# Kernel tuning notes

Hardware: AMD Instinct MI355X
Metric: run time of the kernel (lower is better)

## Reference

```python
import jax, jax.numpy as jnp
import numpy as np

D = 3  # feature dim fixed by the module's Linear(3,3) layers
N = 6144

def _linear(x, w, b):
    # torch Linear: y = x @ W^T + b, W: [out,in]
    return x @ w.T + b

def setup_inputs() -> dict:
    key = jax.random.key(0)
    ks = jax.random.split(key, 20)
    lim = 1.0 / np.sqrt(D)  # torch default init bound
    def W(k):
        return jax.random.uniform(k, (D, D), jnp.float32, -lim, lim)
    def B(k):
        return jax.random.uniform(k, (D,), jnp.float32, -lim, lim)
    inp = {"x_data": jax.random.normal(ks[0], (N, D), jnp.float32)}
    names = ["q1", "q2", "q3", "q4", "k1", "k2", "v1", "v2", "b1b2"]
    for i, nm in enumerate(names):
        inp["w_" + nm] = W(ks[1 + 2 * i])
        inp["b_" + nm] = B(ks[2 + 2 * i])
    return inp

def reference(x_data, w_q1, b_q1, w_q2, b_q2, w_q3, b_q3, w_q4, b_q4,
              w_k1, b_k1, w_k2, b_k2, w_v1, b_v1, w_v2, b_v2, w_b1b2, b_b1b2):
    k1 = _linear(x_data, w_k1, b_k1)
    k2 = _linear(x_data, w_k2, b_k2)
    group1 = _linear(x_data, w_q1, b_q1) + _linear(x_data, w_q2, b_q2)
    group2 = _linear(x_data, w_q3, b_q3) + _linear(x_data, w_q4, b_q4)
    a1 = jax.nn.softmax(group1 @ k1.T, axis=1)  # [N, N]
    a2 = jax.nn.softmax(group2 @ k2.T, axis=1)  # [N, N]
    v1 = _linear(x_data, w_v1, b_v1)
    v2 = _linear(x_data, w_v2, b_v2)
    b = _linear(a1 @ v1 + a2 @ v2, w_b1b2, b_b1b2)  # [N, D]
    return (a1, b)
```

## Files before the change

### kernel.cpp

```cpp
#include <hip/hip_runtime.h>
#include <cstddef>

#define N_ROWS 6144
#define TR 8
#define NT 256
#define NBLK (N_ROWS / TR)
#define JT (NT * 4)
#define NIT (N_ROWS / JT)
#define L2E 1.44269504088896340736f

typedef float f32x4 __attribute__((ext_vector_type(4)));

#if __has_builtin(__builtin_amdgcn_exp2f)
#define EXP2F(x) __builtin_amdgcn_exp2f(x)
#else
#define EXP2F(x) exp2f(x)
#endif
#if __has_builtin(__builtin_amdgcn_logf)
#define LOG2F(x) __builtin_amdgcn_logf(x)
#else
#define LOG2F(x) log2f(x)
#endif

__device__ __forceinline__ float wredSum(float v) {
#pragma unroll
    for (int off = 32; off > 0; off >>= 1) v += __shfl_xor(v, off, 64);
    return v;
}

__global__ __launch_bounds__(NT, 2) void attn_fused(
    const float* __restrict__ x,
    const float* __restrict__ wq1, const float* __restrict__ bq1,
    const float* __restrict__ wq2, const float* __restrict__ bq2,
    const float* __restrict__ wq3, const float* __restrict__ bq3,
    const float* __restrict__ wq4, const float* __restrict__ bq4,
    const float* __restrict__ wk1, const float* __restrict__ bk1,
    const float* __restrict__ wk2, const float* __restrict__ bk2,
    const float* __restrict__ wv1, const float* __restrict__ bv1,
    const float* __restrict__ wv2, const float* __restrict__ bv2,
    const float* __restrict__ wb,  const float* __restrict__ bb,
    float* __restrict__ out)
{
    const int row0 = blockIdx.x * TR;
    const int tid  = threadIdx.x;
    const int wave = tid >> 6;
    const int lane = tid & 63;

    __shared__ float red[4][64];

    float wg1[9], wg2[9], bg1[3], bg2[3];
    float k1w[9], k2w[9], v1w[9], v2w[9];
    float k1b[3], k2b[3], v1b[3], v2b[3];
#pragma unroll
    for (int t = 0; t < 9; t++) {
        wg1[t] = (wq1[t] + wq2[t]) * L2E;
        wg2[t] = (wq3[t] + wq4[t]) * L2E;
        k1w[t] = wk1[t]; k2w[t] = wk2[t];
        v1w[t] = wv1[t]; v2w[t] = wv2[t];
    }
#pragma unroll
    for (int t = 0; t < 3; t++) {
        bg1[t] = (bq1[t] + bq2[t]) * L2E;
        bg2[t] = (bq3[t] + bq4[t]) * L2E;
        k1b[t] = bk1[t]; k2b[t] = bk2[t];
        v1b[t] = bv1[t]; v2b[t] = bv2[t];
    }

    float g1x[TR], g1y[TR], g1z[TR], g2x[TR], g2y[TR], g2z[TR];
#pragma unroll
    for (int r = 0; r < TR; r++) {
        const int i = row0 + r;
        const float x0 = x[3*i+0], x1 = x[3*i+1], x2 = x[3*i+2];
        g1x[r] = wg1[0]*x0 + wg1[1]*x1 + wg1[2]*x2 + bg1[0];
        g1y[r] = wg1[3]*x0 + wg1[4]*x1 + wg1[5]*x2 + bg1[1];
        g1z[r] = wg1[6]*x0 + wg1[7]*x1 + wg1[8]*x2 + bg1[2];
        g2x[r] = wg2[0]*x0 + wg2[1]*x1 + wg2[2]*x2 + bg2[0];
        g2y[r] = wg2[3]*x0 + wg2[4]*x1 + wg2[5]*x2 + bg2[1];
        g2z[r] = wg2[6]*x0 + wg2[7]*x1 + wg2[8]*x2 + bg2[2];
    }

    float l1[TR], l2[TR];
    float o1x[TR], o1y[TR], o1z[TR], o2x[TR], o2y[TR], o2z[TR];
#pragma unroll
    for (int r = 0; r < TR; r++) {
        l1[r]=0.f; l2[r]=0.f;
        o1x[r]=0.f; o1y[r]=0.f; o1z[r]=0.f;
        o2x[r]=0.f; o2y[r]=0.f; o2z[r]=0.f;
    }

    for (int it = 0; it < NIT; it++) {
        const int j0 = it * JT + tid * 4;
        const f32x4 xa = *(const f32x4*)(x + 3*j0);
        const f32x4 xb = *(const f32x4*)(x + 3*j0 + 4);
        const f32x4 xc = *(const f32x4*)(x + 3*j0 + 8);
        const float xs[12] = { xa.x, xa.y, xa.z, xa.w, xb.x, xb.y,
                               xb.z, xb.w, xc.x, xc.y, xc.z, xc.w };
#pragma unroll
        for (int jj = 0; jj < 4; jj++) {
            const float xx = xs[3*jj], xy = xs[3*jj+1], xz = xs[3*jj+2];
            const float k1x = k1w[0]*xx + k1w[1]*xy + k1w[2]*xz + k1b[0];
            const float k1y = k1w[3]*xx + k1w[4]*xy + k1w[5]*xz + k1b[1];
            const float k1z = k1w[6]*xx + k1w[7]*xy + k1w[8]*xz + k1b[2];
            const float k2x = k2w[0]*xx + k2w[1]*xy + k2w[2]*xz + k2b[0];
            const float k2y = k2w[3]*xx + k2w[4]*xy + k2w[5]*xz + k2b[1];
            const float k2z = k2w[6]*xx + k2w[7]*xy + k2w[8]*xz + k2b[2];
            const float v1x = v1w[0]*xx + v1w[1]*xy + v1w[2]*xz + v1b[0];
            const float v1y = v1w[3]*xx + v1w[4]*xy + v1w[5]*xz + v1b[1];
            const float v1z = v1w[6]*xx + v1w[7]*xy + v1w[8]*xz + v1b[2];
            const float v2x = v2w[0]*xx + v2w[1]*xy + v2w[2]*xz + v2b[0];
            const float v2y = v2w[3]*xx + v2w[4]*xy + v2w[5]*xz + v2b[1];
            const float v2z = v2w[6]*xx + v2w[7]*xy + v2w[8]*xz + v2b[2];
#pragma unroll
            for (int r = 0; r < TR; r++) {
                const float t1 = fmaf(g1z[r], k1z, fmaf(g1y[r], k1y, g1x[r]*k1x));
                const float t2 = fmaf(g2z[r], k2z, fmaf(g2y[r], k2y, g2x[r]*k2x));
                const float e1 = EXP2F(t1);
                const float e2 = EXP2F(t2);
                l1[r] += e1; l2[r] += e2;
                o1x[r] = fmaf(e1, v1x, o1x[r]);
                o1y[r] = fmaf(e1, v1y, o1y[r]);
                o1z[r] = fmaf(e1, v1z, o1z[r]);
                o2x[r] = fmaf(e2, v2x, o2x[r]);
                o2y[r] = fmaf(e2, v2y, o2y[r]);
                o2z[r] = fmaf(e2, v2z, o2z[r]);
            }
        }
    }

#pragma unroll
    for (int r = 0; r < TR; r++) {
        l1[r]  = wredSum(l1[r]);  l2[r]  = wredSum(l2[r]);
        o1x[r] = wredSum(o1x[r]); o1y[r] = wredSum(o1y[r]); o1z[r] = wredSum(o1z[r]);
        o2x[r] = wredSum(o2x[r]); o2y[r] = wredSum(o2y[r]); o2z[r] = wredSum(o2z[r]);
        if (lane == 0) {
            red[wave][r*8+0]=l1[r];  red[wave][r*8+1]=l2[r];
            red[wave][r*8+2]=o1x[r]; red[wave][r*8+3]=o1y[r]; red[wave][r*8+4]=o1z[r];
            red[wave][r*8+5]=o2x[r]; red[wave][r*8+6]=o2y[r]; red[wave][r*8+7]=o2z[r];
        }
    }
    __syncthreads();

    float c1p[TR];
#pragma unroll
    for (int r = 0; r < TR; r++) {
        const float l1t = red[0][r*8] + red[1][r*8] + red[2][r*8] + red[3][r*8];
        c1p[r] = -LOG2F(l1t);
    }

    for (int it = 0; it < NIT; it++) {
        const int j0 = it * JT + tid * 4;
        const f32x4 xa = *(const f32x4*)(x + 3*j0);
        const f32x4 xb = *(const f32x4*)(x + 3*j0 + 4);
        const f32x4 xc = *(const f32x4*)(x + 3*j0 + 8);
        const float xs[12] = { xa.x, xa.y, xa.z, xa.w, xb.x, xb.y,
                               xb.z, xb.w, xc.x, xc.y, xc.z, xc.w };
        float K1x[4], K1y[4], K1z[4];
#pragma unroll
        for (int jj = 0; jj < 4; jj++) {
            const float xx = xs[3*jj], xy = xs[3*jj+1], xz = xs[3*jj+2];
            K1x[jj] = k1w[0]*xx + k1w[1]*xy + k1w[2]*xz + k1b[0];
            K1y[jj] = k1w[3]*xx + k1w[4]*xy + k1w[5]*xz + k1b[1];
            K1z[jj] = k1w[6]*xx + k1w[7]*xy + k1w[8]*xz + k1b[2];
        }
#pragma unroll
        for (int r = 0; r < TR; r++) {
            f32x4 pv;
            pv.x = EXP2F(fmaf(g1z[r], K1z[0], fmaf(g1y[r], K1y[0], fmaf(g1x[r], K1x[0], c1p[r]))));
            pv.y = EXP2F(fmaf(g1z[r], K1z[1], fmaf(g1y[r], K1y[1], fmaf(g1x[r], K1x[1], c1p[r]))));
            pv.z = EXP2F(fmaf(g1z[r], K1z[2], fmaf(g1y[r], K1y[2], fmaf(g1x[r], K1x[2], c1p[r]))));
            pv.w = EXP2F(fmaf(g1z[r], K1z[3], fmaf(g1y[r], K1y[3], fmaf(g1x[r], K1x[3], c1p[r]))));
            __builtin_nontemporal_store(pv, (f32x4*)(out + (size_t)(row0 + r) * N_ROWS + j0));
        }
    }

    if (tid < TR) {
        const int r = tid;
        const float l1t = red[0][r*8+0]+red[1][r*8+0]+red[2][r*8+0]+red[3][r*8+0];
        const float l2t = red[0][r*8+1]+red[1][r*8+1]+red[2][r*8+1]+red[3][r*8+1];
        const float sx1 = red[0][r*8+2]+red[1][r*8+2]+red[2][r*8+2]+red[3][r*8+2];
        const float sy1 = red[0][r*8+3]+red[1][r*8+3]+red[2][r*8+3]+red[3][r*8+3];
        const float sz1 = red[0][r*8+4]+red[1][r*8+4]+red[2][r*8+4]+red[3][r*8+4];
        const float sx2 = red[0][r*8+5]+red[1][r*8+5]+red[2][r*8+5]+red[3][r*8+5];
        const float sy2 = red[0][r*8+6]+red[1][r*8+6]+red[2][r*8+6]+red[3][r*8+6];
        const float sz2 = red[0][r*8+7]+red[1][r*8+7]+red[2][r*8+7]+red[3][r*8+7];
        const float r1 = 1.0f / l1t, r2 = 1.0f / l2t;
        const float ox = sx1*r1 + sx2*r2;
        const float oy = sy1*r1 + sy2*r2;
        const float oz = sz1*r1 + sz2*r2;
        const float b0 = wb[0]*ox + wb[1]*oy + wb[2]*oz + bb[0];
        const float b1 = wb[3]*ox + wb[4]*oy + wb[5]*oz + bb[1];
        const float b2 = wb[6]*ox + wb[7]*oy + wb[8]*oz + bb[2];
        const size_t base = (size_t)N_ROWS * N_ROWS + (size_t)(row0 + r) * 3;
        out[base+0] = b0; out[base+1] = b1; out[base+2] = b2;
    }
}

extern "C" void kernel_launch(void* const* d_in, const int* in_sizes, int n_in,
                              void* d_out, int out_size, void* d_ws, size_t ws_size,
                              hipStream_t stream) {
    const float* x   = (const float*)d_in[0];
    const float* wq1 = (const float*)d_in[1];  const float* bq1 = (const float*)d_in[2];
    const float* wq2 = (const float*)d_in[3];  const float* bq2 = (const float*)d_in[4];
    const float* wq3 = (const float*)d_in[5];  const float* bq3 = (const float*)d_in[6];
    const float* wq4 = (const float*)d_in[7];  const float* bq4 = (const float*)d_in[8];
    const float* wk1 = (const float*)d_in[9];  const float* bk1 = (const float*)d_in[10];
    const float* wk2 = (const float*)d_in[11]; const float* bk2 = (const float*)d_in[12];
    const float* wv1 = (const float*)d_in[13]; const float* bv1 = (const float*)d_in[14];
    const float* wv2 = (const float*)d_in[15]; const float* bv2 = (const float*)d_in[16];
    const float* wb  = (const float*)d_in[17]; const float* bb  = (const float*)d_in[18];

    float* out = (float*)d_out;

    attn_fused<<<NBLK, NT, 0, stream>>>(
        x, wq1,bq1, wq2,bq2, wq3,bq3, wq4,bq4,
        wk1,bk1, wk2,bk2, wv1,bv1, wv2,bv2, wb, bb, out);
}
```

Baseline: 220.3 us.

## Split row tile into halves to overlap softmax stores with next-half reduction

Splits each block's 8 rows into two halves of 4. The reduction pass for the second half is fused with writing the normalized attention rows of the first half, so exp-heavy compute and the large nontemporal output stores interleave instead of running in separate phases. Register pressure per loop drops, but x is loaded and K/V recomputed in three passes with less row reuse, and an extra block barrier is added.

```diff
diff --git a/kernel.cpp b/kernel.cpp
--- a/kernel.cpp
+++ b/kernel.cpp
@@ -2,6 +2,7 @@
 #include <cstddef>
 
 #define N_ROWS 6144
+#define TRH 4
 #define TR 8
 #define NT 256
 #define NBLK (N_ROWS / TR)
@@ -46,7 +47,8 @@
     const int wave = tid >> 6;
     const int lane = tid & 63;
 
-    __shared__ float red[4][64];
+    __shared__ float redA[4][TRH * 8];
+    __shared__ float redB[4][TRH * 8];
 
     float wg1[9], wg2[9], bg1[3], bg2[3];
     float k1w[9], k2w[9], v1w[9], v2w[9];
@@ -79,10 +81,10 @@
         g2z[r] = wg2[6]*x0 + wg2[7]*x1 + wg2[8]*x2 + bg2[2];
     }
 
-    float l1[TR], l2[TR];
-    float o1x[TR], o1y[TR], o1z[TR], o2x[TR], o2y[TR], o2z[TR];
-#pragma unroll
-    for (int r = 0; r < TR; r++) {
+    float l1[TRH], l2[TRH];
+    float o1x[TRH], o1y[TRH], o1z[TRH], o2x[TRH], o2y[TRH], o2z[TRH];
+#pragma unroll
+    for (int r = 0; r < TRH; r++) {
         l1[r]=0.f; l2[r]=0.f;
         o1x[r]=0.f; o1y[r]=0.f; o1z[r]=0.f;
         o2x[r]=0.f; o2y[r]=0.f; o2z[r]=0.f;
@@ -111,7 +113,7 @@
             const float v2y = v2w[3]*xx + v2w[4]*xy + v2w[5]*xz + v2b[1];
             const float v2z = v2w[6]*xx + v2w[7]*xy + v2w[8]*xz + v2b[2];
 #pragma unroll
-            for (int r = 0; r < TR; r++) {
+            for (int r = 0; r < TRH; r++) {
                 const float t1 = fmaf(g1z[r], k1z, fmaf(g1y[r], k1y, g1x[r]*k1x));
                 const float t2 = fmaf(g2z[r], k2z, fmaf(g2y[r], k2y, g2x[r]*k2x));
                 const float e1 = EXP2F(t1);
@@ -128,61 +130,35 @@
     }
 
 #pragma unroll
-    for (int r = 0; r < TR; r++) {
+    for (int r = 0; r < TRH; r++) {
         l1[r]  = wredSum(l1[r]);  l2[r]  = wredSum(l2[r]);
         o1x[r] = wredSum(o1x[r]); o1y[r] = wredSum(o1y[r]); o1z[r] = wredSum(o1z[r]);
         o2x[r] = wredSum(o2x[r]); o2y[r] = wredSum(o2y[r]); o2z[r] = wredSum(o2z[r]);
         if (lane == 0) {
-            red[wave][r*8+0]=l1[r];  red[wave][r*8+1]=l2[r];
-            red[wave][r*8+2]=o1x[r]; red[wave][r*8+3]=o1y[r]; red[wave][r*8+4]=o1z[r];
-            red[wave][r*8+5]=o2x[r]; red[wave][r*8+6]=o2y[r]; red[wave][r*8+7]=o2z[r];
+            redA[wave][r*8+0]=l1[r];  redA[wave][r*8+1]=l2[r];
+            redA[wave][r*8+2]=o1x[r]; redA[wave][r*8+3]=o1y[r]; redA[wave][r*8+4]=o1z[r];
+            redA[wave][r*8+5]=o2x[r]; redA[wave][r*8+6]=o2y[r]; redA[wave][r*8+7]=o2z[r];
         }
     }
     __syncthreads();
 
-    float c1p[TR];
-#pragma unroll
-    for (int r = 0; r < TR; r++) {
-        const float l1t = red[0][r*8] + red[1][r*8] + red[2][r*8] + red[3][r*8];
-        c1p[r] = -LOG2F(l1t);
-    }
-
-    for (int it = 0; it < NIT; it++) {
-        const int j0 = it * JT + tid * 4;
-        const f32x4 xa = *(const f32x4*)(x + 3*j0);
-        const f32x4 xb = *(const f32x4*)(x + 3*j0 + 4);
-        const f32x4 xc = *(const f32x4*)(x + 3*j0 + 8);
-        const float xs[12] = { xa.x, xa.y, xa.z, xa.w, xb.x, xb.y,
-                               xb.z, xb.w, xc.x, xc.y, xc.z, xc.w };
-        float K1x[4], K1y[4], K1z[4];
-#pragma unroll
-        for (int jj = 0; jj < 4; jj++) {
-            const float xx = xs[3*jj], xy = xs[3*jj+1], xz = xs[3*jj+2];
-            K1x[jj] = k1w[0]*xx + k1w[1]*xy + k1w[2]*xz + k1b[0];
-            K1y[jj] = k1w[3]*xx + k1w[4]*xy + k1w[5]*xz + k1b[1];
-            K1z[jj] = k1w[6]*xx + k1w[7]*xy + k1w[8]*xz + k1b[2];
-        }
-#pragma unroll
-        for (int r = 0; r < TR; r++) {
-            f32x4 pv;
-            pv.x = EXP2F(fmaf(g1z[r], K1z[0], fmaf(g1y[r], K1y[0], fmaf(g1x[r], K1x[0], c1p[r]))));
-            pv.y = EXP2F(fmaf(g1z[r], K1z[1], fmaf(g1y[r], K1y[1], fmaf(g1x[r], K1x[1], c1p[r]))));
-            pv.z = EXP2F(fmaf(g1z[r], K1z[2], fmaf(g1y[r], K1y[2], fmaf(g1x[r], K1x[2], c1p[r]))));
-            pv.w = EXP2F(fmaf(g1z[r], K1z[3], fmaf(g1y[r], K1y[3], fmaf(g1x[r], K1x[3], c1p[r]))));
-            __builtin_nontemporal_store(pv, (f32x4*)(out + (size_t)(row0 + r) * N_ROWS + j0));
-        }
-    }
-
-    if (tid < TR) {
+    float c1pA[TRH];
+#pragma unroll
+    for (int r = 0; r < TRH; r++) {
+        const float l1t = redA[0][r*8] + redA[1][r*8] + redA[2][r*8] + redA[3][r*8];
+        c1pA[r] = -LOG2F(l1t);
+    }
+
+    if (tid < TRH) {
         const int r = tid;
-        const float l1t = red[0][r*8+0]+red[1][r*8+0]+red[2][r*8+0]+red[3][r*8+0];
-        const float l2t = red[0][r*8+1]+red[1][r*8+1]+red[2][r*8+1]+red[3][r*8+1];
-        const float sx1 = red[0][r*8+2]+red[1][r*8+2]+red[2][r*8+2]+red[3][r*8+2];
-        const float sy1 = red[0][r*8+3]+red[1][r*8+3]+red[2][r*8+3]+red[3][r*8+3];
-        const float sz1 = red[0][r*8+4]+red[1][r*8+4]+red[2][r*8+4]+red[3][r*8+4];
-        const float sx2 = red[0][r*8+5]+red[1][r*8+5]+red[2][r*8+5]+red[3][r*8+5];
-        const float sy2 = red[0][r*8+6]+red[1][r*8+6]+red[2][r*8+6]+red[3][r*8+6];
-        const float sz2 = red[0][r*8+7]+red[1][r*8+7]+red[2][r*8+7]+red[3][r*8+7];
+        const float l1t = redA[0][r*8+0]+redA[1][r*8+0]+redA[2][r*8+0]+redA[3][r*8+0];
+        const float l2t = redA[0][r*8+1]+redA[1][r*8+1]+redA[2][r*8+1]+redA[3][r*8+1];
+        const float sx1 = redA[0][r*8+2]+redA[1][r*8+2]+redA[2][r*8+2]+redA[3][r*8+2];
+        const float sy1 = redA[0][r*8+3]+redA[1][r*8+3]+redA[2][r*8+3]+redA[3][r*8+3];
+        const float sz1 = redA[0][r*8+4]+redA[1][r*8+4]+redA[2][r*8+4]+redA[3][r*8+4];
+        const float sx2 = redA[0][r*8+5]+redA[1][r*8+5]+redA[2][r*8+5]+redA[3][r*8+5];
+        const float sy2 = redA[0][r*8+6]+redA[1][r*8+6]+redA[2][r*8+6]+redA[3][r*8+6];
+        const float sz2 = redA[0][r*8+7]+redA[1][r*8+7]+redA[2][r*8+7]+redA[3][r*8+7];
         const float r1 = 1.0f / l1t, r2 = 1.0f / l2t;
         const float ox = sx1*r1 + sx2*r2;
         const float oy = sy1*r1 + sy2*r2;
@@ -192,6 +168,130 @@
         const float b2 = wb[6]*ox + wb[7]*oy + wb[8]*oz + bb[2];
         const size_t base = (size_t)N_ROWS * N_ROWS + (size_t)(row0 + r) * 3;
         out[base+0] = b0; out[base+1] = b1; out[base+2] = b2;
+    }
+
+#pragma unroll
+    for (int r = 0; r < TRH; r++) {
+        l1[r]=0.f; l2[r]=0.f;
+        o1x[r]=0.f; o1y[r]=0.f; o1z[r]=0.f;
+        o2x[r]=0.f; o2y[r]=0.f; o2z[r]=0.f;
+    }
+
+    for (int it = 0; it < NIT; it++) {
+        const int j0 = it * JT + tid * 4;
+        const f32x4 xa = *(const f32x4*)(x + 3*j0);
+        const f32x4 xb = *(const f32x4*)(x + 3*j0 + 4);
+        const f32x4 xc = *(const f32x4*)(x + 3*j0 + 8);
+        const float xs[12] = { xa.x, xa.y, xa.z, xa.w, xb.x, xb.y,
+                               xb.z, xb.w, xc.x, xc.y, xc.z, xc.w };
+        float K1x[4], K1y[4], K1z[4];
+#pragma unroll
+        for (int jj = 0; jj < 4; jj++) {
+            const float xx = xs[3*jj], xy = xs[3*jj+1], xz = xs[3*jj+2];
+            const float k1x = k1w[0]*xx + k1w[1]*xy + k1w[2]*xz + k1b[0];
+            const float k1y = k1w[3]*xx + k1w[4]*xy + k1w[5]*xz + k1b[1];
+            const float k1z = k1w[6]*xx + k1w[7]*xy + k1w[8]*xz + k1b[2];
+            K1x[jj] = k1x; K1y[jj] = k1y; K1z[jj] = k1z;
+            const float k2x = k2w[0]*xx + k2w[1]*xy + k2w[2]*xz + k2b[0];
+            const float k2y = k2w[3]*xx + k2w[4]*xy + k2w[5]*xz + k2b[1];
+            const float k2z = k2w[6]*xx + k2w[7]*xy + k2w[8]*xz + k2b[2];
+            const float v1x = v1w[0]*xx + v1w[1]*xy + v1w[2]*xz + v1b[0];
+            const float v1y = v1w[3]*xx + v1w[4]*xy + v1w[5]*xz + v1b[1];
+            const float v1z = v1w[6]*xx + v1w[7]*xy + v1w[8]*xz + v1b[2];
+            const float v2x = v2w[0]*xx + v2w[1]*xy + v2w[2]*xz + v2b[0];
+            const float v2y = v2w[3]*xx + v2w[4]*xy + v2w[5]*xz + v2b[1];
+            const float v2z = v2w[6]*xx + v2w[7]*xy + v2w[8]*xz + v2b[2];
+#pragma unroll
+            for (int r = 0; r < TRH; r++) {
+                const float t1 = fmaf(g1z[r+TRH], k1z, fmaf(g1y[r+TRH], k1y, g1x[r+TRH]*k1x));
+                const float t2 = fmaf(g2z[r+TRH], k2z, fmaf(g2y[r+TRH], k2y, g2x[r+TRH]*k2x));
+                const float e1 = EXP2F(t1);
+                const float e2 = EXP2F(t2);
+                l1[r] += e1; l2[r] += e2;
+                o1x[r] = fmaf(e1, v1x, o1x[r]);
+                o1y[r] = fmaf(e1, v1y, o1y[r]);
+                o1z[r] = fmaf(e1, v1z, o1z[r]);
+                o2x[r] = fmaf(e2, v2x, o2x[r]);
+                o2y[r] = fmaf(e2, v2y, o2y[r]);
+                o2z[r] = fmaf(e2, v2z, o2z[r]);
+            }
+        }
+#pragma unroll
+        for (int r = 0; r < TRH; r++) {
+            f32x4 pv;
+            pv.x = EXP2F(fmaf(g1z[r], K1z[0], fmaf(g1y[r], K1y[0], fmaf(g1x[r], K1x[0], c1pA[r]))));
+            pv.y = EXP2F(fmaf(g1z[r], K1z[1], fmaf(g1y[r], K1y[1], fmaf(g1x[r], K1x[1], c1pA[r]))));
+            pv.z = EXP2F(fmaf(g1z[r], K1z[2], fmaf(g1y[r], K1y[2], fmaf(g1x[r], K1x[2], c1pA[r]))));
+            pv.w = EXP2F(fmaf(g1z[r], K1z[3], fmaf(g1y[r], K1y[3], fmaf(g1x[r], K1x[3], c1pA[r]))));
+            __builtin_nontemporal_store(pv, (f32x4*)(out + (size_t)(row0 + r) * N_ROWS + j0));
+        }
+    }
+
+#pragma unroll
+    for (int r = 0; r < TRH; r++) {
+        l1[r]  = wredSum(l1[r]);  l2[r]  = wredSum(l2[r]);
+        o1x[r] = wredSum(o1x[r]); o1y[r] = wredSum(o1y[r]); o1z[r] = wredSum(o1z[r]);
+        o2x[r] = wredSum(o2x[r]); o2y[r] = wredSum(o2y[r]); o2z[r] = wredSum(o2z[r]);
+        if (lane == 0) {
+            redB[wave][r*8+0]=l1[r];  redB[wave][r*8+1]=l2[r];
+            redB[wave][r*8+2]=o1x[r]; redB[wave][r*8+3]=o1y[r]; redB[wave][r*8+4]=o1z[r];
+            redB[wave][r*8+5]=o2x[r]; redB[wave][r*8+6]=o2y[r]; redB[wave][r*8+7]=o2z[r];
+        }
+    }
+    __syncthreads();
+
+    float c1pB[TRH];
+#pragma unroll
+    for (int r = 0; r < TRH; r++) {
+        const float l1t = redB[0][r*8] + redB[1][r*8] + redB[2][r*8] + redB[3][r*8];
+        c1pB[r] = -LOG2F(l1t);
+    }
+
+    if (tid < TRH) {
+        const int r = tid;
+        const float l1t = redB[0][r*8+0]+redB[1][r*8+0]+redB[2][r*8+0]+redB[3][r*8+0];
+        const float l2t = redB[0][r*8+1]+redB[1][r*8+1]+redB[2][r*8+1]+redB[3][r*8+1];
+        const float sx1 = redB[0][r*8+2]+redB[1][r*8+2]+redB[2][r*8+2]+redB[3][r*8+2];
+        const float sy1 = redB[0][r*8+3]+redB[1][r*8+3]+redB[2][r*8+3]+redB[3][r*8+3];
+        const float sz1 = redB[0][r*8+4]+redB[1][r*8+4]+redB[2][r*8+4]+redB[3][r*8+4];
+        const float sx2 = redB[0][r*8+5]+redB[1][r*8+5]+redB[2][r*8+5]+redB[3][r*8+5];
+        const float sy2 = redB[0][r*8+6]+redB[1][r*8+6]+redB[2][r*8+6]+redB[3][r*8+6];
+        const float sz2 = redB[0][r*8+7]+redB[1][r*8+7]+redB[2][r*8+7]+redB[3][r*8+7];
+        const float r1 = 1.0f / l1t, r2 = 1.0f / l2t;
+        const float ox = sx1*r1 + sx2*r2;
+        const float oy = sy1*r1 + sy2*r2;
+        const float oz = sz1*r1 + sz2*r2;
+        const float b0 = wb[0]*ox + wb[1]*oy + wb[2]*oz + bb[0];
+        const float b1 = wb[3]*ox + wb[4]*oy + wb[5]*oz + bb[1];
+        const float b2 = wb[6]*ox + wb[7]*oy + wb[8]*oz + bb[2];
+        const size_t base = (size_t)N_ROWS * N_ROWS + (size_t)(row0 + TRH + r) * 3;
+        out[base+0] = b0; out[base+1] = b1; out[base+2] = b2;
+    }
+
+    for (int it = 0; it < NIT; it++) {
+        const int j0 = it * JT + tid * 4;
+        const f32x4 xa = *(const f32x4*)(x + 3*j0);
+        const f32x4 xb = *(const f32x4*)(x + 3*j0 + 4);
+        const f32x4 xc = *(const f32x4*)(x + 3*j0 + 8);
+        const float xs[12] = { xa.x, xa.y, xa.z, xa.w, xb.x, xb.y,
+                               xb.z, xb.w, xc.x, xc.y, xc.z, xc.w };
+        float K1x[4], K1y[4], K1z[4];
+#pragma unroll
+        for (int jj = 0; jj < 4; jj++) {
+            const float xx = xs[3*jj], xy = xs[3*jj+1], xz = xs[3*jj+2];
+            K1x[jj] = k1w[0]*xx + k1w[1]*xy + k1w[2]*xz + k1b[0];
+            K1y[jj] = k1w[3]*xx + k1w[4]*xy + k1w[5]*xz + k1b[1];
+            K1z[jj] = k1w[6]*xx + k1w[7]*xy + k1w[8]*xz + k1b[2];
+        }
+#pragma unroll
+        for (int r = 0; r < TRH; r++) {
+            f32x4 pv;
+            pv.x = EXP2F(fmaf(g1z[r+TRH], K1z[0], fmaf(g1y[r+TRH], K1y[0], fmaf(g1x[r+TRH], K1x[0], c1pB[r]))));
+            pv.y = EXP2F(fmaf(g1z[r+TRH], K1z[1], fmaf(g1y[r+TRH], K1y[1], fmaf(g1x[r+TRH], K1x[1], c1pB[r]))));
+            pv.z = EXP2F(fmaf(g1z[r+TRH], K1z[2], fmaf(g1y[r+TRH], K1y[2], fmaf(g1x[r+TRH], K1x[2], c1pB[r]))));
+            pv.w = EXP2F(fmaf(g1z[r+TRH], K1z[3], fmaf(g1y[r+TRH], K1y[3], fmaf(g1x[r+TRH], K1x[3], c1pB[r]))));
+            __builtin_nontemporal_store(pv, (f32x4*)(out + (size_t)(row0 + TRH + r) * N_ROWS + j0));
+        }
     }
 }
 
```

After: 224.5 us. No clear change (+1.9%).

## Fold K projection into per-row query and defer V projection to epilogue

Applied to the files above, without the earlier changes.

Precomputes per-row h = Wk^T g and a bias term so that each score is a dot product with raw x, which removes the per-column K projection from both passes. Accumulates softmax-weighted raw x instead of projected V and applies the V weights and bias once per row after normalisation, which relies on softmax weights summing to one. This cuts the per-column FMA work in the inner loops. The cost is slightly different floating-point rounding.

```diff
diff --git a/kernel.cpp b/kernel.cpp
--- a/kernel.cpp
+++ b/kernel.cpp
@@ -66,26 +66,35 @@
         v1b[t] = bv1[t]; v2b[t] = bv2[t];
     }
 
-    float g1x[TR], g1y[TR], g1z[TR], g2x[TR], g2y[TR], g2z[TR];
+    float h1x[TR], h1y[TR], h1z[TR], hc1[TR];
+    float h2x[TR], h2y[TR], h2z[TR], hc2[TR];
 #pragma unroll
     for (int r = 0; r < TR; r++) {
         const int i = row0 + r;
         const float x0 = x[3*i+0], x1 = x[3*i+1], x2 = x[3*i+2];
-        g1x[r] = wg1[0]*x0 + wg1[1]*x1 + wg1[2]*x2 + bg1[0];
-        g1y[r] = wg1[3]*x0 + wg1[4]*x1 + wg1[5]*x2 + bg1[1];
-        g1z[r] = wg1[6]*x0 + wg1[7]*x1 + wg1[8]*x2 + bg1[2];
-        g2x[r] = wg2[0]*x0 + wg2[1]*x1 + wg2[2]*x2 + bg2[0];
-        g2y[r] = wg2[3]*x0 + wg2[4]*x1 + wg2[5]*x2 + bg2[1];
-        g2z[r] = wg2[6]*x0 + wg2[7]*x1 + wg2[8]*x2 + bg2[2];
+        const float g1a = wg1[0]*x0 + wg1[1]*x1 + wg1[2]*x2 + bg1[0];
+        const float g1b = wg1[3]*x0 + wg1[4]*x1 + wg1[5]*x2 + bg1[1];
+        const float g1c = wg1[6]*x0 + wg1[7]*x1 + wg1[8]*x2 + bg1[2];
+        const float g2a = wg2[0]*x0 + wg2[1]*x1 + wg2[2]*x2 + bg2[0];
+        const float g2b = wg2[3]*x0 + wg2[4]*x1 + wg2[5]*x2 + bg2[1];
+        const float g2c = wg2[6]*x0 + wg2[7]*x1 + wg2[8]*x2 + bg2[2];
+        h1x[r] = k1w[0]*g1a + k1w[3]*g1b + k1w[6]*g1c;
+        h1y[r] = k1w[1]*g1a + k1w[4]*g1b + k1w[7]*g1c;
+        h1z[r] = k1w[2]*g1a + k1w[5]*g1b + k1w[8]*g1c;
+        hc1[r] = k1b[0]*g1a + k1b[1]*g1b + k1b[2]*g1c;
+        h2x[r] = k2w[0]*g2a + k2w[3]*g2b + k2w[6]*g2c;
+        h2y[r] = k2w[1]*g2a + k2w[4]*g2b + k2w[7]*g2c;
+        h2z[r] = k2w[2]*g2a + k2w[5]*g2b + k2w[8]*g2c;
+        hc2[r] = k2b[0]*g2a + k2b[1]*g2b + k2b[2]*g2c;
     }
 
     float l1[TR], l2[TR];
-    float o1x[TR], o1y[TR], o1z[TR], o2x[TR], o2y[TR], o2z[TR];
+    float s1x[TR], s1y[TR], s1z[TR], s2x[TR], s2y[TR], s2z[TR];
 #pragma unroll
     for (int r = 0; r < TR; r++) {
         l1[r]=0.f; l2[r]=0.f;
-        o1x[r]=0.f; o1y[r]=0.f; o1z[r]=0.f;
-        o2x[r]=0.f; o2y[r]=0.f; o2z[r]=0.f;
+        s1x[r]=0.f; s1y[r]=0.f; s1z[r]=0.f;
+        s2x[r]=0.f; s2y[r]=0.f; s2z[r]=0.f;
     }
 
     for (int it = 0; it < NIT; it++) {
@@ -98,31 +107,19 @@
 #pragma unroll
         for (int jj = 0; jj < 4; jj++) {
             const float xx = xs[3*jj], xy = xs[3*jj+1], xz = xs[3*jj+2];
-            const float k1x = k1w[0]*xx + k1w[1]*xy + k1w[2]*xz + k1b[0];
-            const float k1y = k1w[3]*xx + k1w[4]*xy + k1w[5]*xz + k1b[1];
-            const float k1z = k1w[6]*xx + k1w[7]*xy + k1w[8]*xz + k1b[2];
-            const float k2x = k2w[0]*xx + k2w[1]*xy + k2w[2]*xz + k2b[0];
-            const float k2y = k2w[3]*xx + k2w[4]*xy + k2w[5]*xz + k2b[1];
-            const float k2z = k2w[6]*xx + k2w[7]*xy + k2w[8]*xz + k2b[2];
-            const float v1x = v1w[0]*xx + v1w[1]*xy + v1w[2]*xz + v1b[0];
-            const float v1y = v1w[3]*xx + v1w[4]*xy + v1w[5]*xz + v1b[1];
-            const float v1z = v1w[6]*xx + v1w[7]*xy + v1w[8]*xz + v1b[2];
-            const float v2x = v2w[0]*xx + v2w[1]*xy + v2w[2]*xz + v2b[0];
-            const float v2y = v2w[3]*xx + v2w[4]*xy + v2w[5]*xz + v2b[1];
-            const float v2z = v2w[6]*xx + v2w[7]*xy + v2w[8]*xz + v2b[2];
 #pragma unroll
             for (int r = 0; r < TR; r++) {
-                const float t1 = fmaf(g1z[r], k1z, fmaf(g1y[r], k1y, g1x[r]*k1x));
-                const float t2 = fmaf(g2z[r], k2z, fmaf(g2y[r], k2y, g2x[r]*k2x));
+                const float t1 = fmaf(h1z[r], xz, fmaf(h1y[r], xy, fmaf(h1x[r], xx, hc1[r])));
+                const float t2 = fmaf(h2z[r], xz, fmaf(h2y[r], xy, fmaf(h2x[r], xx, hc2[r])));
                 const float e1 = EXP2F(t1);
                 const float e2 = EXP2F(t2);
                 l1[r] += e1; l2[r] += e2;
-                o1x[r] = fmaf(e1, v1x, o1x[r]);
-                o1y[r] = fmaf(e1, v1y, o1y[r]);
-                o1z[r] = fmaf(e1, v1z, o1z[r]);
-                o2x[r] = fmaf(e2, v2x, o2x[r]);
-                o2y[r] = fmaf(e2, v2y, o2y[r]);
-                o2z[r] = fmaf(e2, v2z, o2z[r]);
+                s1x[r] = fmaf(e1, xx, s1x[r]);
+                s1y[r] = fmaf(e1, xy, s1y[r]);
+                s1z[r] = fmaf(e1, xz, s1z[r]);
+                s2x[r] = fmaf(e2, xx, s2x[r]);
+                s2y[r] = fmaf(e2, xy, s2y[r]);
+                s2z[r] = fmaf(e2, xz, s2z[r]);
             }
         }
     }
@@ -130,21 +127,21 @@
 #pragma unroll
     for (int r = 0; r < TR; r++) {
         l1[r]  = wredSum(l1[r]);  l2[r]  = wredSum(l2[r]);
-        o1x[r] = wredSum(o1x[r]); o1y[r] = wredSum(o1y[r]); o1z[r] = wredSum(o1z[r]);
-        o2x[r] = wredSum(o2x[r]); o2y[r] = wredSum(o2y[r]); o2z[r] = wredSum(o2z[r]);
+        s1x[r] = wredSum(s1x[r]); s1y[r] = wredSum(s1y[r]); s1z[r] = wredSum(s1z[r]);
+        s2x[r] = wredSum(s2x[r]); s2y[r] = wredSum(s2y[r]); s2z[r] = wredSum(s2z[r]);
         if (lane == 0) {
             red[wave][r*8+0]=l1[r];  red[wave][r*8+1]=l2[r];
-            red[wave][r*8+2]=o1x[r]; red[wave][r*8+3]=o1y[r]; red[wave][r*8+4]=o1z[r];
-            red[wave][r*8+5]=o2x[r]; red[wave][r*8+6]=o2y[r]; red[wave][r*8+7]=o2z[r];
+            red[wave][r*8+2]=s1x[r]; red[wave][r*8+3]=s1y[r]; red[wave][r*8+4]=s1z[r];
+            red[wave][r*8+5]=s2x[r]; red[wave][r*8+6]=s2y[r]; red[wave][r*8+7]=s2z[r];
         }
     }
     __syncthreads();
 
-    float c1p[TR];
+    float cc1[TR];
 #pragma unroll
     for (int r = 0; r < TR; r++) {
         const float l1t = red[0][r*8] + red[1][r*8] + red[2][r*8] + red[3][r*8];
-        c1p[r] = -LOG2F(l1t);
+        cc1[r] = hc1[r] - LOG2F(l1t);
     }
 
     for (int it = 0; it < NIT; it++) {
@@ -154,21 +151,13 @@
         const f32x4 xc = *(const f32x4*)(x + 3*j0 + 8);
         const float xs[12] = { xa.x, xa.y, xa.z, xa.w, xb.x, xb.y,
                                xb.z, xb.w, xc.x, xc.y, xc.z, xc.w };
-        float K1x[4], K1y[4], K1z[4];
-#pragma unroll
-        for (int jj = 0; jj < 4; jj++) {
-            const float xx = xs[3*jj], xy = xs[3*jj+1], xz = xs[3*jj+2];
-            K1x[jj] = k1w[0]*xx + k1w[1]*xy + k1w[2]*xz + k1b[0];
-            K1y[jj] = k1w[3]*xx + k1w[4]*xy + k1w[5]*xz + k1b[1];
-            K1z[jj] = k1w[6]*xx + k1w[7]*xy + k1w[8]*xz + k1b[2];
-        }
 #pragma unroll
         for (int r = 0; r < TR; r++) {
             f32x4 pv;
-            pv.x = EXP2F(fmaf(g1z[r], K1z[0], fmaf(g1y[r], K1y[0], fmaf(g1x[r], K1x[0], c1p[r]))));
-            pv.y = EXP2F(fmaf(g1z[r], K1z[1], fmaf(g1y[r], K1y[1], fmaf(g1x[r], K1x[1], c1p[r]))));
-            pv.z = EXP2F(fmaf(g1z[r], K1z[2], fmaf(g1y[r], K1y[2], fmaf(g1x[r], K1x[2], c1p[r]))));
-            pv.w = EXP2F(fmaf(g1z[r], K1z[3], fmaf(g1y[r], K1y[3], fmaf(g1x[r], K1x[3], c1p[r]))));
+            pv.x = EXP2F(fmaf(h1z[r], xs[2],  fmaf(h1y[r], xs[1],  fmaf(h1x[r], xs[0],  cc1[r]))));
+            pv.y = EXP2F(fmaf(h1z[r], xs[5],  fmaf(h1y[r], xs[4],  fmaf(h1x[r], xs[3],  cc1[r]))));
+            pv.z = EXP2F(fmaf(h1z[r], xs[8],  fmaf(h1y[r], xs[7],  fmaf(h1x[r], xs[6],  cc1[r]))));
+            pv.w = EXP2F(fmaf(h1z[r], xs[11], fmaf(h1y[r], xs[10], fmaf(h1x[r], xs[9],  cc1[r]))));
             __builtin_nontemporal_store(pv, (f32x4*)(out + (size_t)(row0 + r) * N_ROWS + j0));
         }
     }
@@ -177,16 +166,18 @@
         const int r = tid;
         const float l1t = red[0][r*8+0]+red[1][r*8+0]+red[2][r*8+0]+red[3][r*8+0];
         const float l2t = red[0][r*8+1]+red[1][r*8+1]+red[2][r*8+1]+red[3][r*8+1];
-        const float sx1 = red[0][r*8+2]+red[1][r*8+2]+red[2][r*8+2]+red[3][r*8+2];
-        const float sy1 = red[0][r*8+3]+red[1][r*8+3]+red[2][r*8+3]+red[3][r*8+3];
-        const float sz1 = red[0][r*8+4]+red[1][r*8+4]+red[2][r*8+4]+red[3][r*8+4];
-        const float sx2 = red[0][r*8+5]+red[1][r*8+5]+red[2][r*8+5]+red[3][r*8+5];
-        const float sy2 = red[0][r*8+6]+red[1][r*8+6]+red[2][r*8+6]+red[3][r*8+6];
-        const float sz2 = red[0][r*8+7]+red[1][r*8+7]+red[2][r*8+7]+red[3][r*8+7];
-        const float r1 = 1.0f / l1t, r2 = 1.0f / l2t;
-        const float ox = sx1*r1 + sx2*r2;
-        const float oy = sy1*r1 + sy2*r2;
-        const float oz = sz1*r1 + sz2*r2;
+        const float ux1 = (red[0][r*8+2]+red[1][r*8+2]+red[2][r*8+2]+red[3][r*8+2]) / l1t;
+        const float uy1 = (red[0][r*8+3]+red[1][r*8+3]+red[2][r*8+3]+red[3][r*8+3]) / l1t;
+        const float uz1 = (red[0][r*8+4]+red[1][r*8+4]+red[2][r*8+4]+red[3][r*8+4]) / l1t;
+        const float ux2 = (red[0][r*8+5]+red[1][r*8+5]+red[2][r*8+5]+red[3][r*8+5]) / l2t;
+        const float uy2 = (red[0][r*8+6]+red[1][r*8+6]+red[2][r*8+6]+red[3][r*8+6]) / l2t;
+        const float uz2 = (red[0][r*8+7]+red[1][r*8+7]+red[2][r*8+7]+red[3][r*8+7]) / l2t;
+        const float ox = v1w[0]*ux1 + v1w[1]*uy1 + v1w[2]*uz1 + v1b[0]
+                       + v2w[0]*ux2 + v2w[1]*uy2 + v2w[2]*uz2 + v2b[0];
+        const float oy = v1w[3]*ux1 + v1w[4]*uy1 + v1w[5]*uz1 + v1b[1]
+                       + v2w[3]*ux2 + v2w[4]*uy2 + v2w[5]*uz2 + v2b[1];
+        const float oz = v1w[6]*ux1 + v1w[7]*uy1 + v1w[8]*uz1 + v1b[2]
+                       + v2w[6]*ux2 + v2w[7]*uy2 + v2w[8]*uz2 + v2b[2];
         const float b0 = wb[0]*ox + wb[1]*oy + wb[2]*oz + bb[0];
         const float b1 = wb[3]*ox + wb[4]*oy + wb[5]*oz + bb[1];
         const float b2 = wb[6]*ox + wb[7]*oy + wb[8]*oz + bb[2];
```

After: 219.0 us. Within noise of the previous version (-0.6%).
